# Performance work log

Hardware: AMD Instinct MI355X
Metric: run time of the kernel (lower is better)

Reference implementation:

```python
import jax, jax.numpy as jnp
import numpy as np
import math

B, S, D_IN, D_OUT = 4, 2048, 1024, 1024
NEG = -1000000000.0


def setup_inputs() -> dict:
    key = jax.random.key(0)
    ks = jax.random.split(key, 8)
    scale = 1.0 / math.sqrt(D_IN)
    return {
        "x": jax.random.normal(ks[0], (B, S, D_IN), dtype=jnp.float32),
        "Wq": jax.random.normal(ks[1], (D_OUT, D_IN), dtype=jnp.float32) * scale,
        "bq": jax.random.normal(ks[2], (D_OUT,), dtype=jnp.float32) * scale,
        "Wk": jax.random.normal(ks[3], (D_OUT, D_IN), dtype=jnp.float32) * scale,
        "bk": jax.random.normal(ks[4], (D_OUT,), dtype=jnp.float32) * scale,
        "Wv": jax.random.normal(ks[5], (D_OUT, D_IN), dtype=jnp.float32) * scale,
        "bv": jax.random.normal(ks[6], (D_OUT,), dtype=jnp.float32) * scale,
        "lengths": jax.random.randint(ks[7], (B,), 1, S + 1, dtype=jnp.int32),
    }


def reference(x, Wq, bq, Wk, bk, Wv, bv, lengths):
    # QKV projections (self-attention: single input used for q, k, v)
    q = jnp.einsum("bsd,od->bso", x, Wq) + bq
    k = jnp.einsum("bsd,od->bso", x, Wk) + bk
    v = jnp.einsum("bsd,od->bso", x, Wv) + bv
    # scaled scores [B, S, S]
    scores = jnp.einsum("bio,bjo->bij", q, k) / jnp.sqrt(jnp.asarray(D_OUT, q.dtype))
    idx = jnp.arange(S)
    # causal additive mask (mask=True): -1e9 where j > i
    causal = jnp.where(idx[None, :] > idx[:, None], NEG, 0.0).astype(q.dtype)
    # length mask: -1e9 where i >= len[b] or j >= len[b]
    invalid = idx[None, :] >= lengths[:, None]  # [B, S]
    len_mask = jnp.where(invalid[:, :, None] | invalid[:, None, :], NEG, 0.0).astype(q.dtype)
    attn = jax.nn.softmax(scores + causal[None] + len_mask, axis=-1)
    return jnp.einsum("bij,bjo->bio", attn, v)
```

## Files before the change

### kernel.cpp

```cpp
#include <hip/hip_runtime.h>
#include <cstddef>
#include <cstdint>

#define NB 4
#define S_LEN 2048
#define DK 1024

typedef __attribute__((ext_vector_type(8))) short short8;
typedef __attribute__((ext_vector_type(4))) float floatx4;
typedef __attribute__((ext_vector_type(4))) unsigned short ushort4v;
typedef __attribute__((ext_vector_type(8))) unsigned short ushort8v;

__device__ inline unsigned short f2bf(float f) {
    unsigned int u = __float_as_uint(f);
    u += 0x7fff + ((u >> 16) & 1);
    return (unsigned short)(u >> 16);
}
__device__ inline float bf2f(unsigned short u) {
    return __uint_as_float(((unsigned int)u) << 16);
}

#define GLD16(gp, lp)                                                                  \
    __builtin_amdgcn_global_load_lds(                                                  \
        (const __attribute__((address_space(1))) unsigned int*)(gp),                   \
        (__attribute__((address_space(3))) unsigned int*)(lp), 16, 0, 0)

__device__ inline void stage128x64(const unsigned short* __restrict__ g, size_t ld,
                                   unsigned short* __restrict__ lds,
                                   int w, int lane)
{
    const int r8 = lane >> 3;
    const int cg = (lane & 7) ^ r8;
    const unsigned short* gp = g + (size_t)(w * 8 + r8) * ld + cg * 8;
    unsigned short* lp = lds + (size_t)(w * 8) * 64;
    #pragma unroll
    for (int seg = 0; seg < 4; ++seg)
        GLD16(gp + (size_t)(seg * 32) * ld, lp + (size_t)seg * 32 * 64);
}

__global__ __launch_bounds__(256) void cast_all(
    const float* __restrict__ x, const float* __restrict__ Wq,
    const float* __restrict__ Wk, const float* __restrict__ Wv,
    unsigned short* __restrict__ xb, unsigned short* __restrict__ wqb,
    unsigned short* __restrict__ wkb, unsigned short* __restrict__ wvb)
{
    const float* src; unsigned short* dst; int n4;
    if (blockIdx.z == 0)      { src = x;  dst = xb;  n4 = (int)((size_t)NB * S_LEN * DK / 4); }
    else if (blockIdx.z == 1) { src = Wq; dst = wqb; n4 = DK * DK / 4; }
    else if (blockIdx.z == 2) { src = Wk; dst = wkb; n4 = DK * DK / 4; }
    else                      { src = Wv; dst = wvb; n4 = DK * DK / 4; }
    const int stride = gridDim.x * 256;
    for (int i = blockIdx.x * 256 + threadIdx.x; i < n4; i += stride) {
        float4 f = ((const float4*)src)[i];
        ushort4v o;
        o.x = f2bf(f.x); o.y = f2bf(f.y); o.z = f2bf(f.z); o.w = f2bf(f.w);
        ((ushort4v*)dst)[i] = o;
    }
}

__global__ __launch_bounds__(256) void qkv_mfma(
    const unsigned short* __restrict__ xb,
    const unsigned short* __restrict__ wqb, const unsigned short* __restrict__ wkb,
    const unsigned short* __restrict__ wvb,
    const float* __restrict__ bq, const float* __restrict__ bk, const float* __restrict__ bv,
    const int* __restrict__ lengths,
    unsigned short* __restrict__ qb, unsigned short* __restrict__ kb,
    unsigned short* __restrict__ vTb)
{
    __shared__ unsigned short As[128 * 64];
    __shared__ unsigned short Bs[128 * 64];
    const int tid  = threadIdx.x;
    const int w    = tid >> 6, lane = tid & 63;
    const int lm   = lane & 15, quad = lane >> 4;
    const int xr   = lm & 7;
    const int m0   = blockIdx.x * 128, n0 = blockIdx.y * 128;
    const int z    = blockIdx.z;
    const unsigned short* Wb = (z == 0) ? wqb : (z == 1) ? wkb : wvb;
    const float* bias        = (z == 0) ? bq  : (z == 1) ? bk  : bv;

    const int bidx = m0 >> 11;
    const int len  = lengths[bidx];
    const int sm0  = m0 & (S_LEN - 1);
    const bool do_compute = (z == 2) || (sm0 < len);

    const unsigned short* Ag = xb + (size_t)m0 * DK;
    const unsigned short* Bg = Wb + (size_t)n0 * DK;

    const int wr = (w >> 1) * 64, wc = (w & 1) * 64;

    floatx4 acc[4][4];
    #pragma unroll
    for (int r = 0; r < 4; ++r)
        #pragma unroll
        for (int c = 0; c < 4; ++c) acc[r][c] = (floatx4)0.0f;

    if (do_compute) {
        for (int k0 = 0; k0 < DK; k0 += 64) {
            stage128x64(Ag + k0, DK, As, w, lane);
            stage128x64(Bg + k0, DK, Bs, w, lane);
            __syncthreads();
            #pragma unroll
            for (int ks = 0; ks < 2; ++ks) {
                short8 af[4], bf[4];
                #pragma unroll
                for (int r = 0; r < 4; ++r)
                    af[r] = *(const short8*)&As[(size_t)(wr + r*16 + lm) * 64 + ((((ks<<2)|quad) ^ xr) << 3)];
                #pragma unroll
                for (int c = 0; c < 4; ++c)
                    bf[c] = *(const short8*)&Bs[(size_t)(wc + c*16 + lm) * 64 + ((((ks<<2)|quad) ^ xr) << 3)];
                #pragma unroll
                for (int r = 0; r < 4; ++r)
                    #pragma unroll
                    for (int c = 0; c < 4; ++c)
                        acc[r][c] = __builtin_amdgcn_mfma_f32_16x16x32_bf16(af[r], bf[c], acc[r][c], 0, 0, 0);
            }
            __syncthreads();
        }
    }

    if (z < 2) {
        unsigned short* out = (z == 0) ? qb : kb;
        #pragma unroll
        for (int r = 0; r < 4; ++r) {
            const int gm = m0 + wr + r * 16 + quad * 4;
            #pragma unroll
            for (int c = 0; c < 4; ++c) {
                const int gn = n0 + wc + c * 16 + lm;
                const float bb = bias[gn];
                #pragma unroll
                for (int e = 0; e < 4; ++e)
                    out[(size_t)(gm + e) * DK + gn] = f2bf(acc[r][c][e] + bb);
            }
        }
    } else {
        #pragma unroll
        for (int r = 0; r < 4; ++r) {
            const int gm = m0 + wr + r * 16 + quad * 4;
            const int sm = gm & (S_LEN - 1);
            #pragma unroll
            for (int c = 0; c < 4; ++c) {
                const int gn = n0 + wc + c * 16 + lm;
                const float bb = bias[gn];
                ushort4v pk;
                pk.x = f2bf(acc[r][c][0] + bb);
                pk.y = f2bf(acc[r][c][1] + bb);
                pk.z = f2bf(acc[r][c][2] + bb);
                pk.w = f2bf(acc[r][c][3] + bb);
                *(ushort4v*)&vTb[((size_t)bidx * DK + gn) * S_LEN + sm] = pk;
            }
        }
    }
}

__global__ __launch_bounds__(256) void score_mfma(
    const unsigned short* __restrict__ qb, const unsigned short* __restrict__ kb,
    unsigned short* __restrict__ ub, const int* __restrict__ lengths)
{
    const int t = blockIdx.x, b = blockIdx.y;
    int bi = (int)((sqrtf(8.0f * t + 1.0f) - 1.0f) * 0.5f);
    while ((bi + 1) * (bi + 2) / 2 <= t) ++bi;
    while (bi * (bi + 1) / 2 > t) --bi;
    const int bj = t - bi * (bi + 1) / 2;
    const int m0 = bi * 128, n0 = bj * 128;
    const int len = lengths[b];

    __shared__ unsigned short As[128 * 64];
    __shared__ unsigned short Bs[128 * 64];
    const int tid  = threadIdx.x;
    const int w    = tid >> 6, lane = tid & 63;
    const int lm   = lane & 15, quad = lane >> 4;
    const int xr   = lm & 7;
    const unsigned short* Ag = qb + (size_t)b * S_LEN * DK + (size_t)m0 * DK;
    const unsigned short* Bg = kb + (size_t)b * S_LEN * DK + (size_t)n0 * DK;
    unsigned short* Ub = ub + (size_t)b * S_LEN * S_LEN;

    const int wr = (w >> 1) * 64, wc = (w & 1) * 64;

    floatx4 acc[4][4];
    #pragma unroll
    for (int r = 0; r < 4; ++r)
        #pragma unroll
        for (int c = 0; c < 4; ++c) acc[r][c] = (floatx4)0.0f;

    if (m0 < len && n0 < len) {
        for (int k0 = 0; k0 < DK; k0 += 64) {
            stage128x64(Ag + k0, DK, As, w, lane);
            stage128x64(Bg + k0, DK, Bs, w, lane);
            __syncthreads();
            #pragma unroll
            for (int ks = 0; ks < 2; ++ks) {
                short8 af[4], bf[4];
                #pragma unroll
                for (int r = 0; r < 4; ++r)
                    af[r] = *(const short8*)&As[(size_t)(wr + r*16 + lm) * 64 + ((((ks<<2)|quad) ^ xr) << 3)];
                #pragma unroll
                for (int c = 0; c < 4; ++c)
                    bf[c] = *(const short8*)&Bs[(size_t)(wc + c*16 + lm) * 64 + ((((ks<<2)|quad) ^ xr) << 3)];
                #pragma unroll
                for (int r = 0; r < 4; ++r)
                    #pragma unroll
                    for (int c = 0; c < 4; ++c)
                        acc[r][c] = __builtin_amdgcn_mfma_f32_16x16x32_bf16(af[r], bf[c], acc[r][c], 0, 0, 0);
            }
            __syncthreads();
        }
    }

    #pragma unroll
    for (int r = 0; r < 4; ++r) {
        const int gm = m0 + wr + r * 16 + quad * 4;
        #pragma unroll
        for (int c = 0; c < 4; ++c) {
            const int gn = n0 + wc + c * 16 + lm;
            #pragma unroll
            for (int e = 0; e < 4; ++e) {
                const int i = gm + e;
                float u;
                if (gn > i)          u = 0.0f;
                else if (i >= len)   u = 1.0f;
                else                 u = __expf(acc[r][c][e] * 0.03125f);
                Ub[(size_t)i * S_LEN + gn] = f2bf(u);
            }
        }
    }
}

__global__ __launch_bounds__(256) void pv_mfma(
    const unsigned short* __restrict__ ub, const unsigned short* __restrict__ vTb,
    float* __restrict__ out)
{
    __shared__ unsigned short As[128 * 64];
    __shared__ unsigned short Bs[128 * 64];
    __shared__ float sums_lds[128];
    const int tid  = threadIdx.x;
    const int w    = tid >> 6, lane = tid & 63;
    const int lm   = lane & 15, quad = lane >> 4;
    const int xr   = lm & 7;
    const int bi = blockIdx.x, bn = blockIdx.y, b = blockIdx.z;
    const int m0 = bi * 128, n0 = bn * 128;
    const unsigned short* Ag = ub  + (size_t)b * S_LEN * S_LEN + (size_t)m0 * S_LEN;
    const unsigned short* Bg = vTb + (size_t)b * DK * S_LEN    + (size_t)n0 * S_LEN;

    const int wr = (w >> 1) * 64, wc = (w & 1) * 64;
    const int kend = (bi + 1) * 128;

    floatx4 acc[4][4];
    #pragma unroll
    for (int r = 0; r < 4; ++r)
        #pragma unroll
        for (int c = 0; c < 4; ++c) acc[r][c] = (floatx4)0.0f;

    float srow[4] = {0.0f, 0.0f, 0.0f, 0.0f};

    for (int k0 = 0; k0 < kend; k0 += 64) {
        stage128x64(Ag + k0, S_LEN, As, w, lane);
        stage128x64(Bg + k0, S_LEN, Bs, w, lane);
        __syncthreads();
        #pragma unroll
        for (int ks = 0; ks < 2; ++ks) {
            short8 af[4], bf[4];
            #pragma unroll
            for (int r = 0; r < 4; ++r)
                af[r] = *(const short8*)&As[(size_t)(wr + r*16 + lm) * 64 + ((((ks<<2)|quad) ^ xr) << 3)];
            #pragma unroll
            for (int c = 0; c < 4; ++c)
                bf[c] = *(const short8*)&Bs[(size_t)(wc + c*16 + lm) * 64 + ((((ks<<2)|quad) ^ xr) << 3)];
            #pragma unroll
            for (int r = 0; r < 4; ++r) {
                const ushort8v uu = *(const ushort8v*)&af[r];
                #pragma unroll
                for (int e = 0; e < 8; ++e) srow[r] += bf2f(uu[e]);
                #pragma unroll
                for (int c = 0; c < 4; ++c)
                    acc[r][c] = __builtin_amdgcn_mfma_f32_16x16x32_bf16(af[r], bf[c], acc[r][c], 0, 0, 0);
            }
        }
        __syncthreads();
    }

    #pragma unroll
    for (int r = 0; r < 4; ++r) {
        srow[r] += __shfl_xor(srow[r], 16, 64);
        srow[r] += __shfl_xor(srow[r], 32, 64);
    }
    if ((w == 0 || w == 3) && quad == 0) {
        #pragma unroll
        for (int r = 0; r < 4; ++r) sums_lds[wr + r * 16 + lm] = srow[r];
    }
    __syncthreads();

    #pragma unroll
    for (int r = 0; r < 4; ++r) {
        const int lrow = wr + r * 16 + quad * 4;
        const int gm = m0 + lrow;
        float ilv[4];
        #pragma unroll
        for (int e = 0; e < 4; ++e) ilv[e] = 1.0f / sums_lds[lrow + e];
        #pragma unroll
        for (int c = 0; c < 4; ++c) {
            const int gn = n0 + wc + c * 16 + lm;
            #pragma unroll
            for (int e = 0; e < 4; ++e)
                out[((size_t)b * S_LEN + gm + e) * DK + gn] = acc[r][c][e] * ilv[e];
        }
    }
}

extern "C" void kernel_launch(void* const* d_in, const int* in_sizes, int n_in,
                              void* d_out, int out_size, void* d_ws, size_t ws_size,
                              hipStream_t stream)
{
    const float* x  = (const float*)d_in[0];
    const float* Wq = (const float*)d_in[1];
    const float* bq = (const float*)d_in[2];
    const float* Wk = (const float*)d_in[3];
    const float* bk = (const float*)d_in[4];
    const float* Wv = (const float*)d_in[5];
    const float* bv = (const float*)d_in[6];
    const int* lengths = (const int*)d_in[7];
    float* out = (float*)d_out;

    const size_t NQ = (size_t)NB * S_LEN * DK;
    const size_t NW = (size_t)DK * DK;
    unsigned short* ws16 = (unsigned short*)d_ws;
    unsigned short* qb  = ws16;
    unsigned short* kb_ = ws16 + NQ;
    unsigned short* vTb = ws16 + 2 * NQ;
    unsigned short* xb  = ws16 + 3 * NQ;
    unsigned short* wqb = ws16 + 4 * NQ;
    unsigned short* wkb = wqb + NW;
    unsigned short* wvb = wkb + NW;
    unsigned short* ub  = ws16 + 4 * NQ + 3 * NW;

    cast_all<<<dim3(1024, 1, 4), 256, 0, stream>>>(x, Wq, Wk, Wv, xb, wqb, wkb, wvb);
    qkv_mfma<<<dim3(64, 8, 3), 256, 0, stream>>>(xb, wqb, wkb, wvb, bq, bk, bv, lengths,
                                                 qb, kb_, vTb);
    score_mfma<<<dim3(136, NB), 256, 0, stream>>>(qb, kb_, ub, lengths);
    pv_mfma<<<dim3(16, 8, NB), 256, 0, stream>>>(ub, vTb, out);
}
```

Measured before the change: 219.6 us.

## Move softmax row sums into score kernel and narrow PV tiles with reversed order

The score kernel now reduces each 128-row tile's bf16 exponentials into per-row partial sums and writes them to a small workspace buffer. The PV kernel reads those partials instead of accumulating row sums inside its MFMA loop. PV tiles shrink from 128x128 to 128x64 output, doubling the grid, and the heaviest causal row blocks are scheduled first to reduce tail imbalance. The cost is an extra sync, shuffles and global writes in the score kernel, plus twice the re-reads of the U tile in PV.

```diff
diff --git a/kernel.cpp b/kernel.cpp
--- a/kernel.cpp
+++ b/kernel.cpp
@@ -35,6 +35,19 @@
     unsigned short* lp = lds + (size_t)(w * 8) * 64;
     #pragma unroll
     for (int seg = 0; seg < 4; ++seg)
+        GLD16(gp + (size_t)(seg * 32) * ld, lp + (size_t)seg * 32 * 64);
+}
+
+__device__ inline void stage64x64(const unsigned short* __restrict__ g, size_t ld,
+                                  unsigned short* __restrict__ lds,
+                                  int w, int lane)
+{
+    const int r8 = lane >> 3;
+    const int cg = (lane & 7) ^ r8;
+    const unsigned short* gp = g + (size_t)(w * 8 + r8) * ld + cg * 8;
+    unsigned short* lp = lds + (size_t)(w * 8) * 64;
+    #pragma unroll
+    for (int seg = 0; seg < 2; ++seg)
         GLD16(gp + (size_t)(seg * 32) * ld, lp + (size_t)seg * 32 * 64);
 }
 
@@ -154,7 +167,8 @@
 
 __global__ __launch_bounds__(256) void score_mfma(
     const unsigned short* __restrict__ qb, const unsigned short* __restrict__ kb,
-    unsigned short* __restrict__ ub, const int* __restrict__ lengths)
+    unsigned short* __restrict__ ub, float* __restrict__ tsum,
+    const int* __restrict__ lengths)
 {
     const int t = blockIdx.x, b = blockIdx.y;
     int bi = (int)((sqrtf(8.0f * t + 1.0f) - 1.0f) * 0.5f);
@@ -166,6 +180,7 @@
 
     __shared__ unsigned short As[128 * 64];
     __shared__ unsigned short Bs[128 * 64];
+    __shared__ float psum[128][2];
     const int tid  = threadIdx.x;
     const int w    = tid >> 6, lane = tid & 63;
     const int lm   = lane & 15, quad = lane >> 4;
@@ -205,6 +220,13 @@
             __syncthreads();
         }
     }
+    __syncthreads();
+
+    float part[4][4];
+    #pragma unroll
+    for (int r = 0; r < 4; ++r)
+        #pragma unroll
+        for (int e = 0; e < 4; ++e) part[r][e] = 0.0f;
 
     #pragma unroll
     for (int r = 0; r < 4; ++r) {
@@ -219,75 +241,88 @@
                 if (gn > i)          u = 0.0f;
                 else if (i >= len)   u = 1.0f;
                 else                 u = __expf(acc[r][c][e] * 0.03125f);
-                Ub[(size_t)i * S_LEN + gn] = f2bf(u);
-            }
-        }
-    }
+                const unsigned short ub16 = f2bf(u);
+                Ub[(size_t)i * S_LEN + gn] = ub16;
+                part[r][e] += bf2f(ub16);
+            }
+        }
+    }
+
+    #pragma unroll
+    for (int r = 0; r < 4; ++r)
+        #pragma unroll
+        for (int e = 0; e < 4; ++e) {
+            part[r][e] += __shfl_xor(part[r][e], 1, 64);
+            part[r][e] += __shfl_xor(part[r][e], 2, 64);
+            part[r][e] += __shfl_xor(part[r][e], 4, 64);
+            part[r][e] += __shfl_xor(part[r][e], 8, 64);
+        }
+    if (lm == 0) {
+        #pragma unroll
+        for (int r = 0; r < 4; ++r)
+            #pragma unroll
+            for (int e = 0; e < 4; ++e)
+                psum[wr + r * 16 + quad * 4 + e][w & 1] = part[r][e];
+    }
+    __syncthreads();
+    if (tid < 128)
+        tsum[((size_t)b * S_LEN + m0 + tid) * 16 + bj] = psum[tid][0] + psum[tid][1];
 }
 
 __global__ __launch_bounds__(256) void pv_mfma(
     const unsigned short* __restrict__ ub, const unsigned short* __restrict__ vTb,
-    float* __restrict__ out)
+    const float* __restrict__ tsum, float* __restrict__ out)
 {
     __shared__ unsigned short As[128 * 64];
-    __shared__ unsigned short Bs[128 * 64];
-    __shared__ float sums_lds[128];
+    __shared__ unsigned short Bs[64 * 64];
+    __shared__ float inv_lds[128];
     const int tid  = threadIdx.x;
     const int w    = tid >> 6, lane = tid & 63;
     const int lm   = lane & 15, quad = lane >> 4;
     const int xr   = lm & 7;
-    const int bi = blockIdx.x, bn = blockIdx.y, b = blockIdx.z;
-    const int m0 = bi * 128, n0 = bn * 128;
+    const int bi = 15 - blockIdx.x;
+    const int bn = blockIdx.y, b = blockIdx.z;
+    const int m0 = bi * 128, n0 = bn * 64;
     const unsigned short* Ag = ub  + (size_t)b * S_LEN * S_LEN + (size_t)m0 * S_LEN;
     const unsigned short* Bg = vTb + (size_t)b * DK * S_LEN    + (size_t)n0 * S_LEN;
 
-    const int wr = (w >> 1) * 64, wc = (w & 1) * 64;
+    if (tid < 128) {
+        const float* ts = &tsum[((size_t)b * S_LEN + m0 + tid) * 16];
+        float s = 0.0f;
+        for (int j = 0; j <= bi; ++j) s += ts[j];
+        inv_lds[tid] = 1.0f / s;
+    }
+
+    const int wr = (w >> 1) * 64, wc = (w & 1) * 32;
     const int kend = (bi + 1) * 128;
 
-    floatx4 acc[4][4];
-    #pragma unroll
-    for (int r = 0; r < 4; ++r)
-        #pragma unroll
-        for (int c = 0; c < 4; ++c) acc[r][c] = (floatx4)0.0f;
-
-    float srow[4] = {0.0f, 0.0f, 0.0f, 0.0f};
+    floatx4 acc[4][2];
+    #pragma unroll
+    for (int r = 0; r < 4; ++r)
+        #pragma unroll
+        for (int c = 0; c < 2; ++c) acc[r][c] = (floatx4)0.0f;
 
     for (int k0 = 0; k0 < kend; k0 += 64) {
         stage128x64(Ag + k0, S_LEN, As, w, lane);
-        stage128x64(Bg + k0, S_LEN, Bs, w, lane);
+        stage64x64 (Bg + k0, S_LEN, Bs, w, lane);
         __syncthreads();
         #pragma unroll
         for (int ks = 0; ks < 2; ++ks) {
-            short8 af[4], bf[4];
+            short8 af[4], bf[2];
             #pragma unroll
             for (int r = 0; r < 4; ++r)
                 af[r] = *(const short8*)&As[(size_t)(wr + r*16 + lm) * 64 + ((((ks<<2)|quad) ^ xr) << 3)];
             #pragma unroll
-            for (int c = 0; c < 4; ++c)
+            for (int c = 0; c < 2; ++c)
                 bf[c] = *(const short8*)&Bs[(size_t)(wc + c*16 + lm) * 64 + ((((ks<<2)|quad) ^ xr) << 3)];
             #pragma unroll
-            for (int r = 0; r < 4; ++r) {
-                const ushort8v uu = *(const ushort8v*)&af[r];
-                #pragma unroll
-                for (int e = 0; e < 8; ++e) srow[r] += bf2f(uu[e]);
-                #pragma unroll
-                for (int c = 0; c < 4; ++c)
+            for (int r = 0; r < 4; ++r)
+                #pragma unroll
+                for (int c = 0; c < 2; ++c)
                     acc[r][c] = __builtin_amdgcn_mfma_f32_16x16x32_bf16(af[r], bf[c], acc[r][c], 0, 0, 0);
-            }
         }
         __syncthreads();
     }
-
-    #pragma unroll
-    for (int r = 0; r < 4; ++r) {
-        srow[r] += __shfl_xor(srow[r], 16, 64);
-        srow[r] += __shfl_xor(srow[r], 32, 64);
-    }
-    if ((w == 0 || w == 3) && quad == 0) {
-        #pragma unroll
-        for (int r = 0; r < 4; ++r) sums_lds[wr + r * 16 + lm] = srow[r];
-    }
-    __syncthreads();
 
     #pragma unroll
     for (int r = 0; r < 4; ++r) {
@@ -295,9 +330,9 @@
         const int gm = m0 + lrow;
         float ilv[4];
         #pragma unroll
-        for (int e = 0; e < 4; ++e) ilv[e] = 1.0f / sums_lds[lrow + e];
-        #pragma unroll
-        for (int c = 0; c < 4; ++c) {
+        for (int e = 0; e < 4; ++e) ilv[e] = inv_lds[lrow + e];
+        #pragma unroll
+        for (int c = 0; c < 2; ++c) {
             const int gn = n0 + wc + c * 16 + lm;
             #pragma unroll
             for (int e = 0; e < 4; ++e)
@@ -322,6 +357,7 @@
 
     const size_t NQ = (size_t)NB * S_LEN * DK;
     const size_t NW = (size_t)DK * DK;
+    const size_t NP = (size_t)NB * S_LEN * S_LEN;
     unsigned short* ws16 = (unsigned short*)d_ws;
     unsigned short* qb  = ws16;
     unsigned short* kb_ = ws16 + NQ;
@@ -331,10 +367,11 @@
     unsigned short* wkb = wqb + NW;
     unsigned short* wvb = wkb + NW;
     unsigned short* ub  = ws16 + 4 * NQ + 3 * NW;
+    float* tsum = (float*)(ub + NP);
 
     cast_all<<<dim3(1024, 1, 4), 256, 0, stream>>>(x, Wq, Wk, Wv, xb, wqb, wkb, wvb);
     qkv_mfma<<<dim3(64, 8, 3), 256, 0, stream>>>(xb, wqb, wkb, wvb, bq, bk, bv, lengths,
                                                  qb, kb_, vTb);
-    score_mfma<<<dim3(136, NB), 256, 0, stream>>>(qb, kb_, ub, lengths);
-    pv_mfma<<<dim3(16, 8, NB), 256, 0, stream>>>(ub, vTb, out);
-}
+    score_mfma<<<dim3(136, NB), 256, 0, stream>>>(qb, kb_, ub, tsum, lengths);
+    pv_mfma<<<dim3(16, 16, NB), 256, 0, stream>>>(ub, vTb, tsum, out);
+}
```

Measured after the change: 221.6 us. Within noise of the previous version (+0.9%).
